# Performance work log

Measured on AMD Instinct MI355X. Metric: run time of the kernel, lower is better.

Reference implementation:

```python
import jax, jax.numpy as jnp
import numpy as np

B, L, D, V, F = 128, 512, 300, 50000, 1000
FILT = 1  # FILTERS=[1] (uniCNN); FILTER_NUM=[1000]


def setup_inputs() -> dict:
    key = jax.random.key(0)
    ks = jax.random.split(key, 6)
    inp = jax.random.randint(ks[0], (B, L), 0, V)
    emb = jax.random.normal(ks[1], (V, D), jnp.float32) * 0.1
    emb = emb.at[0].set(0.0)  # padding_idx = 0
    conv_w = jax.random.normal(ks[2], (F, 1, D * FILT), jnp.float32) * 0.02
    conv_b = jax.random.normal(ks[3], (F,), jnp.float32) * 0.02
    fc_w = jax.random.normal(ks[4], (2, F), jnp.float32) * 0.02
    fc_b = jax.random.normal(ks[5], (2,), jnp.float32) * 0.02
    return dict(inp=inp, emb=emb, conv_w=conv_w, conv_b=conv_b, fc_w=fc_w, fc_b=fc_b)


def reference(inp, emb, conv_w, conv_b, fc_w, fc_b):
    # Embedding lookup, flattened view [B, 1, D*L] as in the torch module.
    x = emb[inp].reshape(B, 1, D * L)
    # Conv1d: kernel D*FILT, stride D  ->  [B, F, T] with T = L - FILT + 1.
    conv = jax.lax.conv_general_dilated(
        x, conv_w, window_strides=(D,), padding='VALID',
        dimension_numbers=('NCH', 'OIH', 'NCH')) + conv_b[None, :, None]
    act = jax.nn.relu(conv)
    # Max-pool over the full time axis (with indices, as return_indices=True).
    maxpool = jnp.max(act, axis=2)   # [B, F]  (= concat_maxpool; dropout is identity at eval)
    idx = jnp.argmax(act, axis=2)    # [B, F]  position of max in conv output
    # contributions = positive - negative = maxpool * (fc.weight[1] - fc.weight[0])
    contrib = maxpool * (fc_w[1] - fc_w[0])  # [B, F]
    # Vectorized equivalent of the nested-loop scatter_add over filters/offsets.
    token = jnp.zeros((B, L), jnp.float32)
    rows = jnp.arange(B)[:, None]
    for off in range(FILT):  # filter width offsets (FILT=1 here)
        token = token.at[rows, idx + off].add(contrib)
    token = token + (fc_b[1] - fc_b[0])
    return token
```

## Files before the change

### kernel.cpp

```cpp
#include <hip/hip_runtime.h>
#include <math.h>

#define B_ 128
#define L_ 512
#define D_ 300
#define F_ 1000
#define KPAD 320
#define FPAD 1024
#define NKC 10

#define EHI_OFF 0ull
#define ELO_OFF 41943040ull
#define WHI_OFF 83886080ull
#define WLO_OFF 84541440ull
#define WS_NEED 85196800ull

typedef __attribute__((ext_vector_type(8))) short bf16x8;
typedef __attribute__((ext_vector_type(4))) float f32x4;

__device__ __forceinline__ void lds16(const void* g, void* l) {
    __builtin_amdgcn_global_load_lds(
        (const __attribute__((address_space(1))) unsigned int*)g,
        (__attribute__((address_space(3))) unsigned int*)l, 16, 0, 0);
}

__global__ void init_token_kernel(float* __restrict__ out, const float* __restrict__ fc_b) {
    int i = blockIdx.x * blockDim.x + threadIdx.x;
    if (i < B_ * L_) out[i] = fc_b[1] - fc_b[0];
}

__global__ void convert_E(const int* __restrict__ inp, const float* __restrict__ emb,
                          unsigned int* __restrict__ ehi, unsigned int* __restrict__ elo) {
    unsigned gid = blockIdx.x * 256 + threadIdx.x;
    unsigned row = gid / 160u, pr = gid - row * 160u;
    if (row >= 65536u) return;
    const int tok = inp[row];
    const unsigned d = pr * 2u;
    float x = 0.f, y = 0.f;
    if (d < 300u) {
        float2 v = *(const float2*)(emb + (size_t)tok * D_ + d);
        x = v.x; y = v.y;
    }
    const unsigned bx = __float_as_uint(x), by = __float_as_uint(y);
    const unsigned hx = bx & 0xFFFF0000u, hy = by & 0xFFFF0000u;
    const float lx = x - __uint_as_float(hx);
    const float ly = y - __uint_as_float(hy);
    ehi[(size_t)row * 160u + pr] = hy | (bx >> 16);
    elo[(size_t)row * 160u + pr] = (__float_as_uint(ly) & 0xFFFF0000u) | (__float_as_uint(lx) >> 16);
}

__global__ void convert_W(const float* __restrict__ conv_w,
                          unsigned int* __restrict__ whi, unsigned int* __restrict__ wlo) {
    unsigned gid = blockIdx.x * 256 + threadIdx.x;
    unsigned f = gid / 160u, pr = gid - f * 160u;
    if (f >= (unsigned)FPAD) return;
    const unsigned d = pr * 2u;
    float x = 0.f, y = 0.f;
    if (f < (unsigned)F_ && d < 300u) {
        float2 v = *(const float2*)(conv_w + (size_t)f * D_ + d);
        x = v.x; y = v.y;
    }
    const unsigned bx = __float_as_uint(x), by = __float_as_uint(y);
    const unsigned hx = bx & 0xFFFF0000u, hy = by & 0xFFFF0000u;
    const float lx = x - __uint_as_float(hx);
    const float ly = y - __uint_as_float(hy);
    whi[(size_t)f * 160u + pr] = hy | (bx >> 16);
    wlo[(size_t)f * 160u + pr] = (__float_as_uint(ly) & 0xFFFF0000u) | (__float_as_uint(lx) >> 16);
}

__global__ __launch_bounds__(512, 4)
void gemm_max_scatter(const int* __restrict__ inp,
                      const float* __restrict__ emb,
                      const float* __restrict__ conv_w,
                      const float* __restrict__ conv_b,
                      const float* __restrict__ fc_w,
                      const char* __restrict__ ehi, const char* __restrict__ elo,
                      const char* __restrict__ whi, const char* __restrict__ wlo,
                      float* __restrict__ out) {
    __shared__ __align__(16) char smem[73728];
    const int tid  = threadIdx.x;
    const int lane = tid & 63;
    const int w    = tid >> 6;
    const int a    = lane & 15;
    const int h    = lane >> 4;

    const unsigned wg      = blockIdx.x;
    const unsigned logical = (wg & 7u) * 256u + (wg >> 3);
    const int fb    = logical & 15;
    const int b     = logical >> 4;
    const int fBase = fb * 64;

    f32x4 acc[4][4];
#pragma unroll
    for (int mt = 0; mt < 4; ++mt)
#pragma unroll
        for (int nt = 0; nt < 4; ++nt) acc[mt][nt] = (f32x4)(0.f);

    const size_t erow0 = (size_t)b * 512 * KPAD;

    for (int c = 0; c < NKC; ++c) {
        const int d0 = c * 32;
        __syncthreads();
#pragma unroll
        for (int q = 0; q < 4; ++q) {
            const int s = w * 4 + q;
            const size_t src = (erow0 + (size_t)(s * 16 + a) * KPAD + d0 + h * 8) * 2;
            lds16(ehi + src, smem + s * 1024);
            lds16(elo + src, smem + 32768 + s * 1024);
        }
        {
            const int nt = w & 3;
            const size_t src = ((size_t)(fBase + nt * 16 + a) * KPAD + d0 + h * 8) * 2;
            if (w < 4) lds16(whi + src, smem + 65536 + nt * 1024);
            else       lds16(wlo + src, smem + 69632 + nt * 1024);
        }
        asm volatile("s_waitcnt vmcnt(0)" ::: "memory");
        __syncthreads();

        bf16x8 bhi[4], blo[4];
#pragma unroll
        for (int nt = 0; nt < 4; ++nt) {
            bhi[nt] = *(const bf16x8*)(smem + 65536 + nt * 1024 + lane * 16);
            blo[nt] = *(const bf16x8*)(smem + 69632 + nt * 1024 + lane * 16);
        }
#pragma unroll
        for (int mt = 0; mt < 4; ++mt) {
            const int sg = w * 4 + mt;
            const bf16x8 ahi = *(const bf16x8*)(smem + sg * 1024 + lane * 16);
            const bf16x8 alo = *(const bf16x8*)(smem + 32768 + sg * 1024 + lane * 16);
#pragma unroll
            for (int nt = 0; nt < 4; ++nt) {
                acc[mt][nt] = __builtin_amdgcn_mfma_f32_16x16x32_bf16(ahi, bhi[nt], acc[mt][nt], 0, 0, 0);
                acc[mt][nt] = __builtin_amdgcn_mfma_f32_16x16x32_bf16(ahi, blo[nt], acc[mt][nt], 0, 0, 0);
                acc[mt][nt] = __builtin_amdgcn_mfma_f32_16x16x32_bf16(alo, bhi[nt], acc[mt][nt], 0, 0, 0);
            }
        }
    }
    __syncthreads();

    float4* Tup = (float4*)smem;
#pragma unroll
    for (int nt = 0; nt < 4; ++nt) {
        float v1 = -INFINITY, v2 = -INFINITY;
        int   i1 = 0, i2 = 0;
#pragma unroll
        for (int mt = 0; mt < 4; ++mt)
#pragma unroll
            for (int r = 0; r < 4; ++r) {
                const int   t = w * 64 + mt * 16 + h * 4 + r;
                const float v = acc[mt][nt][r];
                if (v > v1)      { v2 = v1; i2 = i1; v1 = v; i1 = t; }
                else if (v > v2) { v2 = v;  i2 = t; }
            }
#pragma unroll
        for (int off = 16; off <= 32; off <<= 1) {
            const float bv1 = __shfl_xor(v1, off);
            const int   bi1 = __shfl_xor(i1, off);
            const float bv2 = __shfl_xor(v2, off);
            const int   bi2 = __shfl_xor(i2, off);
            const bool aTop = (v1 > bv1) || (v1 == bv1 && i1 < bi1);
            float nv1, nv2; int ni1, ni2;
            if (aTop) {
                nv1 = v1; ni1 = i1;
                const bool s = (v2 > bv1) || (v2 == bv1 && i2 < bi1);
                nv2 = s ? v2 : bv1; ni2 = s ? i2 : bi1;
            } else {
                nv1 = bv1; ni1 = bi1;
                const bool s = (bv2 > v1) || (bv2 == v1 && bi2 < i1);
                nv2 = s ? bv2 : v1; ni2 = s ? bi2 : i1;
            }
            v1 = nv1; i1 = ni1; v2 = nv2; i2 = ni2;
        }
        if (lane < 16)
            Tup[w * 64 + nt * 16 + lane] =
                make_float4(v1, __int_as_float(i1), v2, __int_as_float(i2));
    }
    __syncthreads();

#pragma unroll 1
    for (int jj = 0; jj < 8; ++jj) {
        const int fr = w * 8 + jj;
        const int gf = fBase + fr;
        if (gf >= F_) continue;
        float v1 = -INFINITY, v2 = -INFINITY;
        int   i1 = 0, i2 = 0;
#pragma unroll 1
        for (int ww = 0; ww < 8; ++ww) {
            const float4 tp = Tup[ww * 64 + fr];
            const float u1 = tp.x, u2 = tp.z;
            const int   j1 = __float_as_int(tp.y), j2 = __float_as_int(tp.w);
            if (u1 > v1) {
                const bool s = (v1 >= u2);
                v2 = s ? v1 : u2; i2 = s ? i1 : j2;
                v1 = u1; i1 = j1;
            } else if (u1 > v2) { v2 = u1; i2 = j1; }
        }
        const float cb = conv_b[gf];
        const float dw = fc_w[F_ + gf] - fc_w[gf];
        double mv = 0.0; int idx = 0;
        if (v1 - v2 > 1e-4f) {
            mv = (double)v1 + (double)cb; idx = i1;
        } else {
            const float* e1 = emb + (size_t)inp[b * L_ + i1] * D_;
            const float* e2 = emb + (size_t)inp[b * L_ + i2] * D_;
            const float* wf = conv_w + (size_t)gf * D_;
            double p1 = 0.0, p2 = 0.0;
            for (int d = lane; d < D_; d += 64) {
                const double wd = (double)wf[d];
                p1 = fma((double)e1[d], wd, p1);
                p2 = fma((double)e2[d], wd, p2);
            }
            for (int off = 32; off; off >>= 1) {
                p1 += __shfl_down(p1, off);
                p2 += __shfl_down(p2, off);
            }
            const double d1 = p1 + (double)cb, d2 = p2 + (double)cb;
            if (d2 > d1) { mv = d2; idx = i2; }
            else         { mv = d1; idx = i1; }
        }
        if (lane == 0 && mv > 0.0)
            atomicAdd(out + b * L_ + idx, (float)(mv * (double)dw));
    }
}

#define TFo 32
#define DKo 16
#define NCHo 19
__global__ __launch_bounds__(256, 2)
void conv_max_scatter(const int* __restrict__ inp,
                      const float* __restrict__ emb,
                      const float* __restrict__ conv_w,
                      const float* __restrict__ conv_b,
                      const float* __restrict__ fc_w,
                      float* __restrict__ out) {
    __shared__ float E_s[DKo][L_];
    __shared__ float W_s[DKo][TFo + 1];
    __shared__ int   inp_s[L_];
    const int tid = threadIdx.x, b = blockIdx.y, fBase = blockIdx.x * TFo;
    const int lane = tid & 63, wave = tid >> 6, f0 = wave * 8;
    inp_s[tid] = inp[b * L_ + tid];
    inp_s[tid + 256] = inp[b * L_ + tid + 256];
    __syncthreads();
    float acc[8][8];
#pragma unroll
    for (int k = 0; k < 8; ++k)
#pragma unroll
        for (int j = 0; j < 8; ++j) acc[k][j] = 0.f;
    for (int c = 0; c < NCHo; ++c) {
        const int d0 = c * DKo;
#pragma unroll
        for (int e = 0; e < 2; ++e) {
            const int t = tid * 2 + e;
            const float* rowp = emb + (size_t)inp_s[t] * D_ + d0;
#pragma unroll
            for (int s = 0; s < 4; ++s) {
                float4 v;
                if (d0 + s * 4 < D_) v = *(const float4*)(rowp + s * 4);
                else                 v = make_float4(0.f, 0.f, 0.f, 0.f);
                E_s[s * 4 + 0][t] = v.x; E_s[s * 4 + 1][t] = v.y;
                E_s[s * 4 + 2][t] = v.z; E_s[s * 4 + 3][t] = v.w;
            }
        }
#pragma unroll
        for (int e = 0; e < 2; ++e) {
            const int d = tid & 15, f = (tid >> 4) + e * 16, gf = fBase + f;
            float v = 0.f;
            if (gf < F_ && d0 + d < D_) v = conv_w[(size_t)gf * D_ + d0 + d];
            W_s[d][f] = v;
        }
        __syncthreads();
#pragma unroll
        for (int d = 0; d < DKo; ++d) {
            float wv[8], ev[8];
#pragma unroll
            for (int j = 0; j < 8; ++j) wv[j] = W_s[d][f0 + j];
#pragma unroll
            for (int k = 0; k < 8; ++k) ev[k] = E_s[d][lane + 64 * k];
#pragma unroll
            for (int k = 0; k < 8; ++k)
#pragma unroll
                for (int j = 0; j < 8; ++j) acc[k][j] = fmaf(ev[k], wv[j], acc[k][j]);
        }
        __syncthreads();
    }
    float v1a[8], v2a[8]; int i1a[8], i2a[8];
#pragma unroll
    for (int j = 0; j < 8; ++j) {
        float v1 = -INFINITY, v2 = -INFINITY; int i1 = 0, i2 = 0;
#pragma unroll
        for (int k = 0; k < 8; ++k) {
            const int t = lane + 64 * k; const float v = acc[k][j];
            if (v > v1) { v2 = v1; i2 = i1; v1 = v; i1 = t; }
            else if (v > v2) { v2 = v; i2 = t; }
        }
        for (int off = 1; off < 64; off <<= 1) {
            const float bv1 = __shfl_xor(v1, off); const int bi1 = __shfl_xor(i1, off);
            const float bv2 = __shfl_xor(v2, off); const int bi2 = __shfl_xor(i2, off);
            const bool aTop = (v1 > bv1) || (v1 == bv1 && i1 < bi1);
            float nv1, nv2; int ni1, ni2;
            if (aTop) {
                nv1 = v1; ni1 = i1;
                const bool s = (v2 > bv1) || (v2 == bv1 && i2 < bi1);
                nv2 = s ? v2 : bv1; ni2 = s ? i2 : bi1;
            } else {
                nv1 = bv1; ni1 = bi1;
                const bool s = (bv2 > v1) || (bv2 == v1 && bi2 < i1);
                nv2 = s ? bv2 : v1; ni2 = s ? bi2 : i1;
            }
            v1 = nv1; i1 = ni1; v2 = nv2; i2 = ni2;
        }
        v1a[j] = v1; i1a[j] = i1; v2a[j] = v2; i2a[j] = i2;
    }
#pragma unroll 1
    for (int j = 0; j < 8; ++j) {
        const int gf = fBase + f0 + j;
        if (gf >= F_) continue;
        const int i1 = i1a[j], i2 = i2a[j];
        const float* e1 = emb + (size_t)inp_s[i1] * D_;
        const float* e2 = emb + (size_t)inp_s[i2] * D_;
        const float* wf = conv_w + (size_t)gf * D_;
        double p1 = 0.0, p2 = 0.0;
        for (int d = lane; d < D_; d += 64) {
            const double wd = (double)wf[d];
            p1 = fma((double)e1[d], wd, p1);
            p2 = fma((double)e2[d], wd, p2);
        }
        for (int off = 32; off; off >>= 1) { p1 += __shfl_down(p1, off); p2 += __shfl_down(p2, off); }
        if (lane == 0) {
            const double cb = (double)conv_b[gf];
            const double d1 = p1 + cb, d2 = p2 + cb;
            int idx; double mv;
            if (d2 > d1) { idx = i2; mv = d2; } else { idx = i1; mv = d1; }
            if (mv > 0.0)
                atomicAdd(&out[b * L_ + idx], (float)(mv * (double)(fc_w[F_ + gf] - fc_w[gf])));
        }
    }
}

extern "C" void kernel_launch(void* const* d_in, const int* in_sizes, int n_in,
                              void* d_out, int out_size, void* d_ws, size_t ws_size,
                              hipStream_t stream) {
    const int*   inp    = (const int*)d_in[0];
    const float* emb    = (const float*)d_in[1];
    const float* conv_w = (const float*)d_in[2];
    const float* conv_b = (const float*)d_in[3];
    const float* fc_w   = (const float*)d_in[4];
    const float* fc_b   = (const float*)d_in[5];
    float* out = (float*)d_out;

    init_token_kernel<<<dim3((B_ * L_ + 255) / 256), dim3(256), 0, stream>>>(out, fc_b);

    if (ws_size >= WS_NEED) {
        char* ws = (char*)d_ws;
        unsigned int* ehi = (unsigned int*)(ws + EHI_OFF);
        unsigned int* elo = (unsigned int*)(ws + ELO_OFF);
        unsigned int* whi = (unsigned int*)(ws + WHI_OFF);
        unsigned int* wlo = (unsigned int*)(ws + WLO_OFF);
        convert_E<<<dim3(40960), dim3(256), 0, stream>>>(inp, emb, ehi, elo);
        convert_W<<<dim3(640),   dim3(256), 0, stream>>>(conv_w, whi, wlo);
        gemm_max_scatter<<<dim3(2048), dim3(512), 0, stream>>>(
            inp, emb, conv_w, conv_b, fc_w,
            (const char*)ehi, (const char*)elo, (const char*)whi, (const char*)wlo, out);
    } else {
        conv_max_scatter<<<dim3(32, 128), dim3(256), 0, stream>>>(
            inp, emb, conv_w, conv_b, fc_w, out);
    }
}
```

Measured before the change: 405.4 us.

## Double-buffer LDS staging in GEMM loop to overlap loads with MFMA

Doubles the shared-memory buffer and prefetches the next K-chunk of embedding and weight tiles into the alternate buffer while MFMAs run on the current one, dropping one barrier per iteration. LDS use grows to about 144KB per block, so launch bounds fall from 4 to 2 blocks per CU, which may cut occupancy. The near-tie threshold for the exact double-precision recheck of the argmax is also widened from 1e-4 to 4e-4, so more filters take the slower verification path.

Result: slower. 443.1 us (+9.3%).

```diff
diff --git a/kernel.cpp b/kernel.cpp
--- a/kernel.cpp
+++ b/kernel.cpp
@@ -14,6 +14,8 @@
 #define WHI_OFF 83886080ull
 #define WLO_OFF 84541440ull
 #define WS_NEED 85196800ull
+
+#define BUFSZ 73728
 
 typedef __attribute__((ext_vector_type(8))) short bf16x8;
 typedef __attribute__((ext_vector_type(4))) float f32x4;
@@ -68,7 +70,7 @@
     wlo[(size_t)f * 160u + pr] = (__float_as_uint(ly) & 0xFFFF0000u) | (__float_as_uint(lx) >> 16);
 }
 
-__global__ __launch_bounds__(512, 4)
+__global__ __launch_bounds__(512, 2)
 void gemm_max_scatter(const int* __restrict__ inp,
                       const float* __restrict__ emb,
                       const float* __restrict__ conv_w,
@@ -77,7 +79,7 @@
                       const char* __restrict__ ehi, const char* __restrict__ elo,
                       const char* __restrict__ whi, const char* __restrict__ wlo,
                       float* __restrict__ out) {
-    __shared__ __align__(16) char smem[73728];
+    __shared__ __align__(16) char smem[2 * BUFSZ];
     const int tid  = threadIdx.x;
     const int lane = tid & 63;
     const int w    = tid >> 6;
@@ -97,37 +99,43 @@
         for (int nt = 0; nt < 4; ++nt) acc[mt][nt] = (f32x4)(0.f);
 
     const size_t erow0 = (size_t)b * 512 * KPAD;
+    const int    ntB   = w & 3;
+
+#define STAGE(c_, buf_)                                                          \
+    {                                                                            \
+        const int d0_ = (c_) * 32;                                               \
+        _Pragma("unroll")                                                        \
+        for (int q = 0; q < 4; ++q) {                                            \
+            const int s = w * 4 + q;                                             \
+            const size_t src = (erow0 + (size_t)(s * 16 + a) * KPAD + d0_ + h * 8) * 2; \
+            lds16(ehi + src, (buf_) + s * 1024);                                 \
+            lds16(elo + src, (buf_) + 32768 + s * 1024);                         \
+        }                                                                        \
+        const size_t srcB = ((size_t)(fBase + ntB * 16 + a) * KPAD + d0_ + h * 8) * 2;  \
+        if (w < 4) lds16(whi + srcB, (buf_) + 65536 + ntB * 1024);               \
+        else       lds16(wlo + srcB, (buf_) + 69632 + ntB * 1024);               \
+    }
+
+    STAGE(0, smem);
 
     for (int c = 0; c < NKC; ++c) {
-        const int d0 = c * 32;
-        __syncthreads();
-#pragma unroll
-        for (int q = 0; q < 4; ++q) {
-            const int s = w * 4 + q;
-            const size_t src = (erow0 + (size_t)(s * 16 + a) * KPAD + d0 + h * 8) * 2;
-            lds16(ehi + src, smem + s * 1024);
-            lds16(elo + src, smem + 32768 + s * 1024);
-        }
-        {
-            const int nt = w & 3;
-            const size_t src = ((size_t)(fBase + nt * 16 + a) * KPAD + d0 + h * 8) * 2;
-            if (w < 4) lds16(whi + src, smem + 65536 + nt * 1024);
-            else       lds16(wlo + src, smem + 69632 + nt * 1024);
-        }
+        char* cur = smem + (c & 1) * BUFSZ;
+        char* nxt = smem + ((c + 1) & 1) * BUFSZ;
         asm volatile("s_waitcnt vmcnt(0)" ::: "memory");
         __syncthreads();
+        if (c + 1 < NKC) STAGE(c + 1, nxt);
 
         bf16x8 bhi[4], blo[4];
 #pragma unroll
         for (int nt = 0; nt < 4; ++nt) {
-            bhi[nt] = *(const bf16x8*)(smem + 65536 + nt * 1024 + lane * 16);
-            blo[nt] = *(const bf16x8*)(smem + 69632 + nt * 1024 + lane * 16);
+            bhi[nt] = *(const bf16x8*)(cur + 65536 + nt * 1024 + lane * 16);
+            blo[nt] = *(const bf16x8*)(cur + 69632 + nt * 1024 + lane * 16);
         }
 #pragma unroll
         for (int mt = 0; mt < 4; ++mt) {
             const int sg = w * 4 + mt;
-            const bf16x8 ahi = *(const bf16x8*)(smem + sg * 1024 + lane * 16);
-            const bf16x8 alo = *(const bf16x8*)(smem + 32768 + sg * 1024 + lane * 16);
+            const bf16x8 ahi = *(const bf16x8*)(cur + sg * 1024 + lane * 16);
+            const bf16x8 alo = *(const bf16x8*)(cur + 32768 + sg * 1024 + lane * 16);
 #pragma unroll
             for (int nt = 0; nt < 4; ++nt) {
                 acc[mt][nt] = __builtin_amdgcn_mfma_f32_16x16x32_bf16(ahi, bhi[nt], acc[mt][nt], 0, 0, 0);
@@ -198,7 +206,7 @@
         const float cb = conv_b[gf];
         const float dw = fc_w[F_ + gf] - fc_w[gf];
         double mv = 0.0; int idx = 0;
-        if (v1 - v2 > 1e-4f) {
+        if (v1 - v2 > 4e-4f) {
             mv = (double)v1 + (double)cb; idx = i1;
         } else {
             const float* e1 = emb + (size_t)inp[b * L_ + i1] * D_;
@@ -221,6 +229,7 @@
         if (lane == 0 && mv > 0.0)
             atomicAdd(out + b * L_ + idx, (float)(mv * (double)dw));
     }
+#undef STAGE
 }
 
 #define TFo 32
```

## Load A operands directly to registers and ring-buffer B tiles in LDS

Applied to the files above, without the earlier changes.

The embedding (A) fragments are now loaded straight from global memory into registers instead of staged through LDS. Only the weight (B) tiles go through a 4-slot LDS ring buffer with one-chunk prefetch, synchronised by a partial vmcnt wait and a single barrier per K chunk. This cuts LDS usage from 72KB to 32KB, which may allow more resident workgroups, and removes one of the two barriers per K chunk. The argmax tie threshold is also widened, which sends more filters to the double-precision recheck path.

Result: faster. 386.5 us (-4.7%).

```diff
diff --git a/kernel.cpp b/kernel.cpp
--- a/kernel.cpp
+++ b/kernel.cpp
@@ -77,7 +77,7 @@
                       const char* __restrict__ ehi, const char* __restrict__ elo,
                       const char* __restrict__ whi, const char* __restrict__ wlo,
                       float* __restrict__ out) {
-    __shared__ __align__(16) char smem[73728];
+    __shared__ __align__(16) char smem[4 * 8192];
     const int tid  = threadIdx.x;
     const int lane = tid & 63;
     const int w    = tid >> 6;
@@ -97,42 +97,43 @@
         for (int nt = 0; nt < 4; ++nt) acc[mt][nt] = (f32x4)(0.f);
 
     const size_t erow0 = (size_t)b * 512 * KPAD;
+    const int    ntB   = w & 3;
+
+    const size_t aoff = (erow0 + (size_t)(w * 64 + a) * KPAD + h * 8) * 2;
+    const char* pAhi = ehi + aoff;
+    const char* pAlo = elo + aoff;
+    const char* pBsrc = (w < 4 ? whi : wlo) +
+                        ((size_t)(fBase + ntB * 16 + a) * KPAD + h * 8) * 2;
+    const int   bdst  = (w < 4 ? 0 : 4096) + ntB * 1024;
+
+    lds16(pBsrc, smem + bdst);
 
     for (int c = 0; c < NKC; ++c) {
-        const int d0 = c * 32;
-        __syncthreads();
-#pragma unroll
-        for (int q = 0; q < 4; ++q) {
-            const int s = w * 4 + q;
-            const size_t src = (erow0 + (size_t)(s * 16 + a) * KPAD + d0 + h * 8) * 2;
-            lds16(ehi + src, smem + s * 1024);
-            lds16(elo + src, smem + 32768 + s * 1024);
-        }
-        {
-            const int nt = w & 3;
-            const size_t src = ((size_t)(fBase + nt * 16 + a) * KPAD + d0 + h * 8) * 2;
-            if (w < 4) lds16(whi + src, smem + 65536 + nt * 1024);
-            else       lds16(wlo + src, smem + 69632 + nt * 1024);
-        }
-        asm volatile("s_waitcnt vmcnt(0)" ::: "memory");
-        __syncthreads();
-
-        bf16x8 bhi[4], blo[4];
+        const int coff = c * 64;
+        bf16x8 ahi[4], alo[4];
+#pragma unroll
+        for (int mt = 0; mt < 4; ++mt)
+            ahi[mt] = *(const bf16x8*)(pAhi + mt * 10240 + coff);
+#pragma unroll
+        for (int mt = 0; mt < 4; ++mt)
+            alo[mt] = *(const bf16x8*)(pAlo + mt * 10240 + coff);
+        if (c + 1 < NKC) {
+            lds16(pBsrc + coff + 64, smem + (((c + 1) & 3) * 8192) + bdst);
+            asm volatile("s_waitcnt vmcnt(9)" ::: "memory");
+        } else {
+            asm volatile("s_waitcnt vmcnt(8)" ::: "memory");
+        }
+        asm volatile("s_barrier" ::: "memory");
+        const char* bs = smem + (c & 3) * 8192;
 #pragma unroll
         for (int nt = 0; nt < 4; ++nt) {
-            bhi[nt] = *(const bf16x8*)(smem + 65536 + nt * 1024 + lane * 16);
-            blo[nt] = *(const bf16x8*)(smem + 69632 + nt * 1024 + lane * 16);
-        }
-#pragma unroll
-        for (int mt = 0; mt < 4; ++mt) {
-            const int sg = w * 4 + mt;
-            const bf16x8 ahi = *(const bf16x8*)(smem + sg * 1024 + lane * 16);
-            const bf16x8 alo = *(const bf16x8*)(smem + 32768 + sg * 1024 + lane * 16);
-#pragma unroll
-            for (int nt = 0; nt < 4; ++nt) {
-                acc[mt][nt] = __builtin_amdgcn_mfma_f32_16x16x32_bf16(ahi, bhi[nt], acc[mt][nt], 0, 0, 0);
-                acc[mt][nt] = __builtin_amdgcn_mfma_f32_16x16x32_bf16(ahi, blo[nt], acc[mt][nt], 0, 0, 0);
-                acc[mt][nt] = __builtin_amdgcn_mfma_f32_16x16x32_bf16(alo, bhi[nt], acc[mt][nt], 0, 0, 0);
+            const bf16x8 bh = *(const bf16x8*)(bs + nt * 1024 + lane * 16);
+            const bf16x8 bl = *(const bf16x8*)(bs + 4096 + nt * 1024 + lane * 16);
+#pragma unroll
+            for (int mt = 0; mt < 4; ++mt) {
+                acc[mt][nt] = __builtin_amdgcn_mfma_f32_16x16x32_bf16(ahi[mt], bh, acc[mt][nt], 0, 0, 0);
+                acc[mt][nt] = __builtin_amdgcn_mfma_f32_16x16x32_bf16(ahi[mt], bl, acc[mt][nt], 0, 0, 0);
+                acc[mt][nt] = __builtin_amdgcn_mfma_f32_16x16x32_bf16(alo[mt], bh, acc[mt][nt], 0, 0, 0);
             }
         }
     }
@@ -198,7 +199,7 @@
         const float cb = conv_b[gf];
         const float dw = fc_w[F_ + gf] - fc_w[gf];
         double mv = 0.0; int idx = 0;
-        if (v1 - v2 > 1e-4f) {
+        if (v1 - v2 > 4e-4f) {
             mv = (double)v1 + (double)cb; idx = i1;
         } else {
             const float* e1 = emb + (size_t)inp[b * L_ + i1] * D_;
```
